# Optimization experiments

Measured on AMD Instinct MI355X. Metric: run time of the kernel, lower is better.

The kernel has to match this reference:

```python
import jax, jax.numpy as jnp
import numpy as np

NODE_NUM = 65536
HID = 256
NUM_CLASS = 64
N_TAB0, N_TAB1 = 40000, 30000
S0, S1 = 8, 4


def setup_inputs() -> dict:
    key = jax.random.key(0)
    ks = jax.random.split(key, 9)
    scale = 1.0 / np.sqrt(HID)
    return {
        "h0": jax.random.normal(ks[0], (NODE_NUM, HID), jnp.float32),
        "tab0": jax.random.normal(ks[1], (N_TAB0, HID), jnp.float32),
        "tab1": jax.random.normal(ks[2], (N_TAB1, HID), jnp.float32),
        "idx0": jax.random.randint(ks[3], (NODE_NUM, S0), 0, N_TAB0, jnp.int32),
        "idx1": jax.random.randint(ks[4], (NODE_NUM, S1), 0, N_TAB1, jnp.int32),
        "W1": jax.random.normal(ks[5], (HID, HID), jnp.float32) * scale,
        "b1": jnp.zeros((HID,), jnp.float32),
        "W2": jax.random.normal(ks[6], (HID, NUM_CLASS), jnp.float32) * scale,
        "b2": jnp.zeros((NUM_CLASS,), jnp.float32),
        "alpha": jax.random.normal(ks[7], (NODE_NUM, 1), jnp.float32),
    }


def _mlp(x, W1, b1, W2, b2):
    # MLP2 with num_layers=2, dropout=0 (eval): relu(x@W1+b1)@W2+b2
    h = jax.nn.relu(jnp.einsum("...i,ij->...j", x, W1) + b1)
    return jnp.einsum("...h,hc->...c", h, W2) + b2


def reference(h0, tab0, tab1, idx0, idx1, W1, b1, W2, b2, alpha):
    # per-type: gather sampled neighbor embeds, MLP, exp(log_softmax)=softmax, mean over samples
    def one_type(tab, idx):
        emb = tab[idx]                                  # [N, S, HID] irregular gather
        cls = jax.nn.softmax(_mlp(emb, W1, b1, W2, b2), axis=-1)  # [N, S, C]
        return jnp.mean(cls, axis=1)                    # [N, C]

    nei_cls = 0.5 * (one_type(tab0, idx0) + one_type(tab1, idx1))
    node_cls = jax.nn.softmax(_mlp(h0, W1, b1, W2, b2), axis=-1)  # [N, C]
    a = jax.nn.sigmoid(alpha)                          # sigmoid(-alpha) = 1 - sigmoid(alpha)
    return a * node_cls + (1.0 - a) * nei_cls
```

## Files before the change

### kernel.cpp

```cpp
#include <hip/hip_runtime.h>

#define HID 256
#define NCLS 64
#define N_NODE 65536
#define N_TAB0 40000
#define N_TAB1 30000
#define S0 8
#define S1 4
#define TILES 2
#define TOTROWS (N_TAB0 + N_TAB1 + N_NODE)
#define PBUF 16384

typedef __attribute__((ext_vector_type(8))) _Float16 f16x8;
typedef __attribute__((ext_vector_type(4))) float f32x4;

__device__ __forceinline__ unsigned short f32_to_h(float x) {
  _Float16 h = (_Float16)x;
  return __builtin_bit_cast(unsigned short, h);
}
__device__ __forceinline__ unsigned pack2h(float lo, float hi) {
  return (unsigned)f32_to_h(lo) | ((unsigned)f32_to_h(hi) << 16);
}

__global__ void prep_kernel(const float* __restrict__ W1, const float* __restrict__ W2,
                            unsigned short* __restrict__ w1f, unsigned short* __restrict__ w2f) {
  int t = blockIdx.x * blockDim.x + threadIdx.x;
  if (t < HID * HID) {
    int j = t & 7, l = (t >> 3) & 63, kt = (t >> 9) & 7, nt = t >> 12;
    w1f[t] = f32_to_h(W1[(kt * 32 + (l >> 4) * 8 + j) * HID + nt * 16 + (l & 15)]);
  } else {
    int t2 = t - HID * HID;
    if (t2 < HID * NCLS) {
      int j = t2 & 7, l = (t2 >> 3) & 63, kt = (t2 >> 9) & 7, ct = t2 >> 12;
      w2f[t2] = f32_to_h(W2[(kt * 32 + (l >> 4) * 8 + j) * NCLS + ct * 16 + (l & 15)]);
    }
  }
}

__launch_bounds__(256, 2)
__global__ void mlp_all_kernel(const float* __restrict__ tab0, const float* __restrict__ tab1,
                               const float* __restrict__ h0,
                               const unsigned short* __restrict__ w1f,
                               const float* __restrict__ b1,
                               const unsigned short* __restrict__ w2f,
                               const float* __restrict__ b2,
                               float* __restrict__ cls0, float* __restrict__ cls1,
                               float* __restrict__ out,
                               const float* __restrict__ alpha) {
  __shared__ __align__(16) char Wlds[2 * PBUF];

  const int t = threadIdx.x;
  const int lane = t & 63;
  const int wv = t >> 6;
  const int nr = lane & 15;
  const int u = lane >> 4;
  const int base = (blockIdx.x * 4 + wv) * (TILES * 16);
  const int lo16 = lane * 16;

  auto STAGE = [&](int pair, int bsel) {
    char* dst = Wlds + bsel * PBUF;
#pragma unroll
    for (int i = 0; i < 4; ++i) {
      const int q = wv * 4 + i;
      const unsigned short* src = w1f + (size_t)(pair * 16 + q) * 512;
      __builtin_amdgcn_global_load_lds(
          (const __attribute__((address_space(1))) void*)(src + lane * 8),
          (__attribute__((address_space(3))) void*)(dst + q * 1024), 16, 0, 0);
    }
  };

  STAGE(0, 0);

  f16x8 bx[TILES][8];
#pragma unroll
  for (int tl = 0; tl < TILES; ++tl) {
    const int row = base + tl * 16 + nr;
    const float* src;
    int lrow;
    if (row < N_TAB0) { src = tab0; lrow = row; }
    else if (row < N_TAB0 + N_TAB1) { src = tab1; lrow = row - N_TAB0; }
    else { src = h0; lrow = row - (N_TAB0 + N_TAB1); }
    const bool rok = (row < TOTROWS);
    const float* xrow = src + (size_t)lrow * HID;
#pragma unroll
    for (int kt = 0; kt < 8; ++kt) {
      float xv[8];
      if (rok) {
        float4 a = *(const float4*)&xrow[kt * 32 + u * 8];
        float4 b = *(const float4*)&xrow[kt * 32 + u * 8 + 4];
        xv[0] = a.x; xv[1] = a.y; xv[2] = a.z; xv[3] = a.w;
        xv[4] = b.x; xv[5] = b.y; xv[6] = b.z; xv[7] = b.w;
      } else {
#pragma unroll
        for (int j = 0; j < 8; ++j) xv[j] = 0.f;
      }
      f16x8 pk;
#pragma unroll
      for (int j = 0; j < 8; ++j) pk[j] = (_Float16)xv[j];
      bx[tl][kt] = pk;
    }
  }

  f32x4 lg[TILES][4];
#pragma unroll
  for (int ct = 0; ct < 4; ++ct) {
    float4 bv = *(const float4*)&b2[ct * 16 + u * 4];
#pragma unroll
    for (int tl = 0; tl < TILES; ++tl) {
      lg[tl][ct][0] = bv.x; lg[tl][ct][1] = bv.y;
      lg[tl][ct][2] = bv.z; lg[tl][ct][3] = bv.w;
    }
  }

  const f16x8* W2F = (const f16x8*)w2f;

  int addr[4];
#pragma unroll
  for (int m = 0; m < 4; ++m) addr[m] = (nr + 16 * (2 * (u & 1) + (m >> 1))) * 4;
  const bool useOdd = (u >= 2);

  auto slice = [&](int nt, unsigned* P0, unsigned* P1) {
    const char* wb = Wlds + ((nt >> 1) & 1) * PBUF + (nt & 1) * 8192;
    f32x4 ae[TILES], ao[TILES];
    float4 bv = *(const float4*)&b1[nt * 16 + u * 4];
#pragma unroll
    for (int tl = 0; tl < TILES; ++tl) {
      ae[tl][0] = bv.x; ae[tl][1] = bv.y; ae[tl][2] = bv.z; ae[tl][3] = bv.w;
      ao[tl][0] = 0.f;  ao[tl][1] = 0.f;  ao[tl][2] = 0.f;  ao[tl][3] = 0.f;
    }
#pragma unroll
    for (int kt = 0; kt < 8; kt += 2) {
      f16x8 ah0 = *(const f16x8*)(wb + kt * 1024 + lo16);
      f16x8 ah1 = *(const f16x8*)(wb + (kt + 1) * 1024 + lo16);
#pragma unroll
      for (int tl = 0; tl < TILES; ++tl) {
        ae[tl] = __builtin_amdgcn_mfma_f32_16x16x32_f16(ah0, bx[tl][kt], ae[tl], 0, 0, 0);
        ao[tl] = __builtin_amdgcn_mfma_f32_16x16x32_f16(ah1, bx[tl][kt + 1], ao[tl], 0, 0, 0);
      }
    }
#pragma unroll
    for (int tl = 0; tl < TILES; ++tl) {
      P0[tl] = pack2h(fmaxf(ae[tl][0] + ao[tl][0], 0.f), fmaxf(ae[tl][1] + ao[tl][1], 0.f));
      P1[tl] = pack2h(fmaxf(ae[tl][2] + ao[tl][2], 0.f), fmaxf(ae[tl][3] + ao[tl][3], 0.f));
    }
  };

  __syncthreads();

  for (int kt2 = 0; kt2 < 8; ++kt2) {
    if (kt2 + 1 < 8) STAGE(kt2 + 1, (kt2 + 1) & 1);

    f16x8 aw[4];
#pragma unroll
    for (int ct = 0; ct < 4; ++ct) aw[ct] = W2F[(ct * 8 + kt2) * 64 + lane];

    unsigned E0[TILES], E1[TILES], O0[TILES], O1[TILES];
    slice(kt2 * 2, E0, E1);
    slice(kt2 * 2 + 1, O0, O1);

    f16x8 bh[TILES];
#pragma unroll
    for (int tl = 0; tl < TILES; ++tl) {
      union { unsigned d[4]; f16x8 v; } r;
#pragma unroll
      for (int m = 0; m < 4; ++m) {
        int e = __builtin_amdgcn_ds_bpermute(addr[m], (int)((m & 1) ? E1[tl] : E0[tl]));
        int o = __builtin_amdgcn_ds_bpermute(addr[m], (int)((m & 1) ? O1[tl] : O0[tl]));
        r.d[m] = (unsigned)(useOdd ? o : e);
      }
      bh[tl] = r.v;
    }

#pragma unroll
    for (int ct = 0; ct < 4; ++ct) {
#pragma unroll
      for (int tl = 0; tl < TILES; ++tl) {
        lg[tl][ct] = __builtin_amdgcn_mfma_f32_16x16x32_f16(aw[ct], bh[tl], lg[tl][ct], 0, 0, 0);
      }
    }

    if (kt2 + 1 < 8) __syncthreads();
  }

#pragma unroll
  for (int tl = 0; tl < TILES; ++tl) {
    const int row = base + tl * 16 + nr;
    float m = lg[tl][0][0];
#pragma unroll
    for (int ct = 0; ct < 4; ++ct)
#pragma unroll
      for (int r = 0; r < 4; ++r) m = fmaxf(m, lg[tl][ct][r]);
    m = fmaxf(m, __shfl_xor(m, 16, 64));
    m = fmaxf(m, __shfl_xor(m, 32, 64));
    float p[4][4];
    float s = 0.f;
#pragma unroll
    for (int ct = 0; ct < 4; ++ct)
#pragma unroll
      for (int r = 0; r < 4; ++r) { p[ct][r] = __expf(lg[tl][ct][r] - m); s += p[ct][r]; }
    s += __shfl_xor(s, 16, 64);
    s += __shfl_xor(s, 32, 64);
    float inv = 1.f / s;

    float* dst;
    int lrow;
    if (row < N_TAB0) { dst = cls0; lrow = row; }
    else if (row < N_TAB0 + N_TAB1) { dst = cls1; lrow = row - N_TAB0; }
    else {
      dst = out; lrow = row - (N_TAB0 + N_TAB1);
      if (row < TOTROWS) inv *= 1.f / (1.f + __expf(-alpha[lrow]));
    }

    if (row < TOTROWS) {
#pragma unroll
      for (int ct = 0; ct < 4; ++ct) {
        float4 o;
        o.x = p[ct][0] * inv; o.y = p[ct][1] * inv;
        o.z = p[ct][2] * inv; o.w = p[ct][3] * inv;
        *(float4*)&dst[(size_t)lrow * NCLS + ct * 16 + u * 4] = o;
      }
    }
  }
}

__launch_bounds__(256)
__global__ void blend_kernel(const float* __restrict__ cls0, const float* __restrict__ cls1,
                             const int* __restrict__ idx0, const int* __restrict__ idx1,
                             const float* __restrict__ alpha, float* __restrict__ out) {
  const int t = threadIdx.x;
  const int lane = t & 63;
  const int wv = t >> 6;
  const int g = lane >> 4;
  const int q = lane & 15;
  const int n = blockIdx.x * 16 + wv * 4 + g;

  int4 ia = *(const int4*)&idx0[n * S0];
  int4 ib = *(const int4*)&idx0[n * S0 + 4];
  int4 ic = *(const int4*)&idx1[n * S1];
  const int j0[S0] = {ia.x, ia.y, ia.z, ia.w, ib.x, ib.y, ib.z, ib.w};
  const int j1[S1] = {ic.x, ic.y, ic.z, ic.w};

  float4 s0 = make_float4(0.f, 0.f, 0.f, 0.f);
#pragma unroll
  for (int k = 0; k < S0; ++k) {
    float4 gv = *(const float4*)&cls0[(size_t)j0[k] * NCLS + q * 4];
    s0.x += gv.x; s0.y += gv.y; s0.z += gv.z; s0.w += gv.w;
  }
  float4 s1 = make_float4(0.f, 0.f, 0.f, 0.f);
#pragma unroll
  for (int k = 0; k < S1; ++k) {
    float4 gv = *(const float4*)&cls1[(size_t)j1[k] * NCLS + q * 4];
    s1.x += gv.x; s1.y += gv.y; s1.z += gv.z; s1.w += gv.w;
  }

  const float a = 1.f / (1.f + __expf(-alpha[n]));
  const float w = (1.f - a) * 0.5f;
  const float c0 = w * (1.f / S0);
  const float c1 = w * (1.f / S1);

  float* op = &out[(size_t)n * NCLS + q * 4];
  float4 o = *(const float4*)op;
  o.x += c0 * s0.x + c1 * s1.x;
  o.y += c0 * s0.y + c1 * s1.y;
  o.z += c0 * s0.z + c1 * s1.z;
  o.w += c0 * s0.w + c1 * s1.w;
  *(float4*)op = o;
}

extern "C" void kernel_launch(void* const* d_in, const int* in_sizes, int n_in,
                              void* d_out, int out_size, void* d_ws, size_t ws_size,
                              hipStream_t stream) {
  const float* h0    = (const float*)d_in[0];
  const float* tab0  = (const float*)d_in[1];
  const float* tab1  = (const float*)d_in[2];
  const int*   idx0  = (const int*)d_in[3];
  const int*   idx1  = (const int*)d_in[4];
  const float* W1    = (const float*)d_in[5];
  const float* b1    = (const float*)d_in[6];
  const float* W2    = (const float*)d_in[7];
  const float* b2    = (const float*)d_in[8];
  const float* alpha = (const float*)d_in[9];
  float* out = (float*)d_out;

  char* ws = (char*)d_ws;
  float* cls0 = (float*)ws;
  float* cls1 = (float*)(ws + 10240000);
  unsigned short* w1f = (unsigned short*)(ws + 17920000);
  unsigned short* w2f = (unsigned short*)(ws + 18051072);

  prep_kernel<<<(HID * HID + HID * NCLS) / 256, 256, 0, stream>>>(W1, W2, w1f, w2f);

  const int RPB = 4 * TILES * 16;
  mlp_all_kernel<<<(TOTROWS + RPB - 1) / RPB, 256, 0, stream>>>(
      tab0, tab1, h0, w1f, b1, w2f, b2, cls0, cls1, out, alpha);

  blend_kernel<<<N_NODE / 16, 256, 0, stream>>>(cls0, cls1, idx0, idx1, alpha, out);
}
```

Before: 90.39 us.

## Stage full W1 in LDS once per 1024-thread block, drop double-buffered pipeline

The MLP kernel now uses 1024-thread blocks with 16 waves, each handling one 16-row tile. The whole fp16 W1 (128 KB) is loaded into LDS once up front, replacing the per-step double-buffered staging and the barriers inside the loop. The goal is to spread each W1 load over more rows and remove the barrier after every step. In exchange, each wave keeps only one tile of rows, so fewer MFMAs run per LDS weight read. The 128 KB of LDS also limits residency to one block per CU, and no loads overlap the compute.

```diff
diff --git a/kernel.cpp b/kernel.cpp
--- a/kernel.cpp
+++ b/kernel.cpp
@@ -7,9 +7,9 @@
 #define N_TAB1 30000
 #define S0 8
 #define S1 4
-#define TILES 2
+#define WAVES 16
+#define TILES 1
 #define TOTROWS (N_TAB0 + N_TAB1 + N_NODE)
-#define PBUF 16384
 
 typedef __attribute__((ext_vector_type(8))) _Float16 f16x8;
 typedef __attribute__((ext_vector_type(4))) float f32x4;
@@ -37,7 +37,7 @@
   }
 }
 
-__launch_bounds__(256, 2)
+__launch_bounds__(1024, 1)
 __global__ void mlp_all_kernel(const float* __restrict__ tab0, const float* __restrict__ tab1,
                                const float* __restrict__ h0,
                                const unsigned short* __restrict__ w1f,
@@ -47,34 +47,27 @@
                                float* __restrict__ cls0, float* __restrict__ cls1,
                                float* __restrict__ out,
                                const float* __restrict__ alpha) {
-  __shared__ __align__(16) char Wlds[2 * PBUF];
+  __shared__ __align__(16) char Wlds[131072];
 
   const int t = threadIdx.x;
   const int lane = t & 63;
   const int wv = t >> 6;
   const int nr = lane & 15;
   const int u = lane >> 4;
-  const int base = (blockIdx.x * 4 + wv) * (TILES * 16);
+  const int base = (blockIdx.x * WAVES + wv) * 16;
   const int lo16 = lane * 16;
 
-  auto STAGE = [&](int pair, int bsel) {
-    char* dst = Wlds + bsel * PBUF;
-#pragma unroll
-    for (int i = 0; i < 4; ++i) {
-      const int q = wv * 4 + i;
-      const unsigned short* src = w1f + (size_t)(pair * 16 + q) * 512;
-      __builtin_amdgcn_global_load_lds(
-          (const __attribute__((address_space(1))) void*)(src + lane * 8),
-          (__attribute__((address_space(3))) void*)(dst + q * 1024), 16, 0, 0);
-    }
-  };
-
-  STAGE(0, 0);
-
-  f16x8 bx[TILES][8];
-#pragma unroll
-  for (int tl = 0; tl < TILES; ++tl) {
-    const int row = base + tl * 16 + nr;
+#pragma unroll
+  for (int i = 0; i < 8; ++i) {
+    const int q = wv * 8 + i;
+    __builtin_amdgcn_global_load_lds(
+        (const __attribute__((address_space(1))) void*)(w1f + (size_t)q * 512 + lane * 8),
+        (__attribute__((address_space(3))) void*)(Wlds + q * 1024), 16, 0, 0);
+  }
+
+  f16x8 bx[8];
+  {
+    const int row = base + nr;
     const float* src;
     int lrow;
     if (row < N_TAB0) { src = tab0; lrow = row; }
@@ -97,19 +90,15 @@
       f16x8 pk;
 #pragma unroll
       for (int j = 0; j < 8; ++j) pk[j] = (_Float16)xv[j];
-      bx[tl][kt] = pk;
-    }
-  }
-
-  f32x4 lg[TILES][4];
+      bx[kt] = pk;
+    }
+  }
+
+  f32x4 lg[4];
 #pragma unroll
   for (int ct = 0; ct < 4; ++ct) {
     float4 bv = *(const float4*)&b2[ct * 16 + u * 4];
-#pragma unroll
-    for (int tl = 0; tl < TILES; ++tl) {
-      lg[tl][ct][0] = bv.x; lg[tl][ct][1] = bv.y;
-      lg[tl][ct][2] = bv.z; lg[tl][ct][3] = bv.w;
-    }
+    lg[ct][0] = bv.x; lg[ct][1] = bv.y; lg[ct][2] = bv.z; lg[ct][3] = bv.w;
   }
 
   const f16x8* W2F = (const f16x8*)w2f;
@@ -120,76 +109,58 @@
   const bool useOdd = (u >= 2);
 
   auto slice = [&](int nt, unsigned* P0, unsigned* P1) {
-    const char* wb = Wlds + ((nt >> 1) & 1) * PBUF + (nt & 1) * 8192;
-    f32x4 ae[TILES], ao[TILES];
+    const char* wb = Wlds + nt * 8192;
+    f32x4 ae, ao;
     float4 bv = *(const float4*)&b1[nt * 16 + u * 4];
-#pragma unroll
-    for (int tl = 0; tl < TILES; ++tl) {
-      ae[tl][0] = bv.x; ae[tl][1] = bv.y; ae[tl][2] = bv.z; ae[tl][3] = bv.w;
-      ao[tl][0] = 0.f;  ao[tl][1] = 0.f;  ao[tl][2] = 0.f;  ao[tl][3] = 0.f;
-    }
+    ae[0] = bv.x; ae[1] = bv.y; ae[2] = bv.z; ae[3] = bv.w;
+    ao[0] = 0.f;  ao[1] = 0.f;  ao[2] = 0.f;  ao[3] = 0.f;
 #pragma unroll
     for (int kt = 0; kt < 8; kt += 2) {
       f16x8 ah0 = *(const f16x8*)(wb + kt * 1024 + lo16);
       f16x8 ah1 = *(const f16x8*)(wb + (kt + 1) * 1024 + lo16);
-#pragma unroll
-      for (int tl = 0; tl < TILES; ++tl) {
-        ae[tl] = __builtin_amdgcn_mfma_f32_16x16x32_f16(ah0, bx[tl][kt], ae[tl], 0, 0, 0);
-        ao[tl] = __builtin_amdgcn_mfma_f32_16x16x32_f16(ah1, bx[tl][kt + 1], ao[tl], 0, 0, 0);
-      }
-    }
-#pragma unroll
-    for (int tl = 0; tl < TILES; ++tl) {
-      P0[tl] = pack2h(fmaxf(ae[tl][0] + ao[tl][0], 0.f), fmaxf(ae[tl][1] + ao[tl][1], 0.f));
-      P1[tl] = pack2h(fmaxf(ae[tl][2] + ao[tl][2], 0.f), fmaxf(ae[tl][3] + ao[tl][3], 0.f));
-    }
+      ae = __builtin_amdgcn_mfma_f32_16x16x32_f16(ah0, bx[kt], ae, 0, 0, 0);
+      ao = __builtin_amdgcn_mfma_f32_16x16x32_f16(ah1, bx[kt + 1], ao, 0, 0, 0);
+    }
+    *P0 = pack2h(fmaxf(ae[0] + ao[0], 0.f), fmaxf(ae[1] + ao[1], 0.f));
+    *P1 = pack2h(fmaxf(ae[2] + ao[2], 0.f), fmaxf(ae[3] + ao[3], 0.f));
   };
 
   __syncthreads();
 
   for (int kt2 = 0; kt2 < 8; ++kt2) {
-    if (kt2 + 1 < 8) STAGE(kt2 + 1, (kt2 + 1) & 1);
-
     f16x8 aw[4];
 #pragma unroll
     for (int ct = 0; ct < 4; ++ct) aw[ct] = W2F[(ct * 8 + kt2) * 64 + lane];
 
-    unsigned E0[TILES], E1[TILES], O0[TILES], O1[TILES];
-    slice(kt2 * 2, E0, E1);
-    slice(kt2 * 2 + 1, O0, O1);
-
-    f16x8 bh[TILES];
-#pragma unroll
-    for (int tl = 0; tl < TILES; ++tl) {
+    unsigned E0, E1, O0, O1;
+    slice(kt2 * 2, &E0, &E1);
+    slice(kt2 * 2 + 1, &O0, &O1);
+
+    f16x8 bh;
+    {
       union { unsigned d[4]; f16x8 v; } r;
 #pragma unroll
       for (int m = 0; m < 4; ++m) {
-        int e = __builtin_amdgcn_ds_bpermute(addr[m], (int)((m & 1) ? E1[tl] : E0[tl]));
-        int o = __builtin_amdgcn_ds_bpermute(addr[m], (int)((m & 1) ? O1[tl] : O0[tl]));
+        int e = __builtin_amdgcn_ds_bpermute(addr[m], (int)((m & 1) ? E1 : E0));
+        int o = __builtin_amdgcn_ds_bpermute(addr[m], (int)((m & 1) ? O1 : O0));
         r.d[m] = (unsigned)(useOdd ? o : e);
       }
-      bh[tl] = r.v;
+      bh = r.v;
     }
 
 #pragma unroll
     for (int ct = 0; ct < 4; ++ct) {
-#pragma unroll
-      for (int tl = 0; tl < TILES; ++tl) {
-        lg[tl][ct] = __builtin_amdgcn_mfma_f32_16x16x32_f16(aw[ct], bh[tl], lg[tl][ct], 0, 0, 0);
-      }
-    }
-
-    if (kt2 + 1 < 8) __syncthreads();
-  }
-
-#pragma unroll
-  for (int tl = 0; tl < TILES; ++tl) {
-    const int row = base + tl * 16 + nr;
-    float m = lg[tl][0][0];
+      lg[ct] = __builtin_amdgcn_mfma_f32_16x16x32_f16(aw[ct], bh, lg[ct], 0, 0, 0);
+    }
+  }
+
+  {
+    const int row = base + nr;
+    float m = lg[0][0];
 #pragma unroll
     for (int ct = 0; ct < 4; ++ct)
 #pragma unroll
-      for (int r = 0; r < 4; ++r) m = fmaxf(m, lg[tl][ct][r]);
+      for (int r = 0; r < 4; ++r) m = fmaxf(m, lg[ct][r]);
     m = fmaxf(m, __shfl_xor(m, 16, 64));
     m = fmaxf(m, __shfl_xor(m, 32, 64));
     float p[4][4];
@@ -197,7 +168,7 @@
 #pragma unroll
     for (int ct = 0; ct < 4; ++ct)
 #pragma unroll
-      for (int r = 0; r < 4; ++r) { p[ct][r] = __expf(lg[tl][ct][r] - m); s += p[ct][r]; }
+      for (int r = 0; r < 4; ++r) { p[ct][r] = __expf(lg[ct][r] - m); s += p[ct][r]; }
     s += __shfl_xor(s, 16, 64);
     s += __shfl_xor(s, 32, 64);
     float inv = 1.f / s;
@@ -290,8 +261,8 @@
 
   prep_kernel<<<(HID * HID + HID * NCLS) / 256, 256, 0, stream>>>(W1, W2, w1f, w2f);
 
-  const int RPB = 4 * TILES * 16;
-  mlp_all_kernel<<<(TOTROWS + RPB - 1) / RPB, 256, 0, stream>>>(
+  const int RPB = WAVES * TILES * 16;
+  mlp_all_kernel<<<(TOTROWS + RPB - 1) / RPB, 1024, 0, stream>>>(
       tab0, tab1, h0, w1f, b1, w2f, b2, cls0, cls1, out, alpha);
 
   blend_kernel<<<N_NODE / 16, 256, 0, stream>>>(cls0, cls1, idx0, idx1, alpha, out);
```

Measured after the change: 106.6 us. 1.18x slower.

## Stage W1 in four-slice groups and issue bpermutes between slice MFMAs

Applied to the files above, without the earlier changes.

W1 is now staged into LDS in groups of four 16-column slices, using two 32KB buffers instead of two 16KB ones. This halves the number of block-wide barriers in the main loop and fully unrolls it. The even-slice ds_bpermute shuffles are issued before the odd-slice MFMAs so the LDS permute latency can overlap with matrix work. The cost is doubled LDS (64KB per block), which may limit occupancy against the 2-blocks-per-CU launch bound, and extra register pressure from the unrolling.

```diff
diff --git a/kernel.cpp b/kernel.cpp
--- a/kernel.cpp
+++ b/kernel.cpp
@@ -9,7 +9,7 @@
 #define S1 4
 #define TILES 2
 #define TOTROWS (N_TAB0 + N_TAB1 + N_NODE)
-#define PBUF 16384
+#define QBUF 32768
 
 typedef __attribute__((ext_vector_type(8))) _Float16 f16x8;
 typedef __attribute__((ext_vector_type(4))) float f32x4;
@@ -47,7 +47,7 @@
                                float* __restrict__ cls0, float* __restrict__ cls1,
                                float* __restrict__ out,
                                const float* __restrict__ alpha) {
-  __shared__ __align__(16) char Wlds[2 * PBUF];
+  __shared__ __align__(16) char Wlds[2 * QBUF];
 
   const int t = threadIdx.x;
   const int lane = t & 63;
@@ -57,19 +57,19 @@
   const int base = (blockIdx.x * 4 + wv) * (TILES * 16);
   const int lo16 = lane * 16;
 
-  auto STAGE = [&](int pair, int bsel) {
-    char* dst = Wlds + bsel * PBUF;
-#pragma unroll
-    for (int i = 0; i < 4; ++i) {
-      const int q = wv * 4 + i;
-      const unsigned short* src = w1f + (size_t)(pair * 16 + q) * 512;
+  auto STAGE4 = [&](int grp, int bsel) {
+    char* dst = Wlds + bsel * QBUF;
+#pragma unroll
+    for (int i = 0; i < 8; ++i) {
+      const int q = wv * 8 + i;
+      const unsigned short* src = w1f + (size_t)(grp * 32 + q) * 512;
       __builtin_amdgcn_global_load_lds(
           (const __attribute__((address_space(1))) void*)(src + lane * 8),
           (__attribute__((address_space(3))) void*)(dst + q * 1024), 16, 0, 0);
     }
   };
 
-  STAGE(0, 0);
+  STAGE4(0, 0);
 
   f16x8 bx[TILES][8];
 #pragma unroll
@@ -120,7 +120,7 @@
   const bool useOdd = (u >= 2);
 
   auto slice = [&](int nt, unsigned* P0, unsigned* P1) {
-    const char* wb = Wlds + ((nt >> 1) & 1) * PBUF + (nt & 1) * 8192;
+    const char* wb = Wlds + ((nt >> 2) & 1) * QBUF + (nt & 3) * 8192;
     f32x4 ae[TILES], ao[TILES];
     float4 bv = *(const float4*)&b1[nt * 16 + u * 4];
 #pragma unroll
@@ -147,39 +147,55 @@
 
   __syncthreads();
 
-  for (int kt2 = 0; kt2 < 8; ++kt2) {
-    if (kt2 + 1 < 8) STAGE(kt2 + 1, (kt2 + 1) & 1);
-
-    f16x8 aw[4];
-#pragma unroll
-    for (int ct = 0; ct < 4; ++ct) aw[ct] = W2F[(ct * 8 + kt2) * 64 + lane];
-
-    unsigned E0[TILES], E1[TILES], O0[TILES], O1[TILES];
-    slice(kt2 * 2, E0, E1);
-    slice(kt2 * 2 + 1, O0, O1);
-
-    f16x8 bh[TILES];
-#pragma unroll
-    for (int tl = 0; tl < TILES; ++tl) {
-      union { unsigned d[4]; f16x8 v; } r;
-#pragma unroll
-      for (int m = 0; m < 4; ++m) {
-        int e = __builtin_amdgcn_ds_bpermute(addr[m], (int)((m & 1) ? E1[tl] : E0[tl]));
-        int o = __builtin_amdgcn_ds_bpermute(addr[m], (int)((m & 1) ? O1[tl] : O0[tl]));
-        r.d[m] = (unsigned)(useOdd ? o : e);
-      }
-      bh[tl] = r.v;
-    }
-
-#pragma unroll
-    for (int ct = 0; ct < 4; ++ct) {
+#pragma unroll
+  for (int g = 0; g < 4; ++g) {
+    if (g + 1 < 4) STAGE4(g + 1, (g + 1) & 1);
+
+#pragma unroll
+    for (int h = 0; h < 2; ++h) {
+      const int kt2 = g * 2 + h;
+
+      f16x8 aw[4];
+#pragma unroll
+      for (int ct = 0; ct < 4; ++ct) aw[ct] = W2F[(ct * 8 + kt2) * 64 + lane];
+
+      unsigned E0[TILES], E1[TILES], O0[TILES], O1[TILES];
+      slice(kt2 * 2, E0, E1);
+
+      int eb[TILES][4];
+#pragma unroll
+      for (int tl = 0; tl < TILES; ++tl)
+#pragma unroll
+        for (int m = 0; m < 4; ++m)
+          eb[tl][m] = __builtin_amdgcn_ds_bpermute(addr[m], (int)((m & 1) ? E1[tl] : E0[tl]));
+
+      slice(kt2 * 2 + 1, O0, O1);
+
+      int ob[TILES][4];
+#pragma unroll
+      for (int tl = 0; tl < TILES; ++tl)
+#pragma unroll
+        for (int m = 0; m < 4; ++m)
+          ob[tl][m] = __builtin_amdgcn_ds_bpermute(addr[m], (int)((m & 1) ? O1[tl] : O0[tl]));
+
+      f16x8 bh[TILES];
 #pragma unroll
       for (int tl = 0; tl < TILES; ++tl) {
-        lg[tl][ct] = __builtin_amdgcn_mfma_f32_16x16x32_f16(aw[ct], bh[tl], lg[tl][ct], 0, 0, 0);
-      }
-    }
-
-    if (kt2 + 1 < 8) __syncthreads();
+        union { unsigned d[4]; f16x8 v; } r;
+#pragma unroll
+        for (int m = 0; m < 4; ++m) r.d[m] = (unsigned)(useOdd ? ob[tl][m] : eb[tl][m]);
+        bh[tl] = r.v;
+      }
+#pragma unroll
+      for (int ct = 0; ct < 4; ++ct) {
+#pragma unroll
+        for (int tl = 0; tl < TILES; ++tl) {
+          lg[tl][ct] = __builtin_amdgcn_mfma_f32_16x16x32_f16(aw[ct], bh[tl], lg[tl][ct], 0, 0, 0);
+        }
+      }
+    }
+
+    if (g + 1 < 4) __syncthreads();
   }
 
 #pragma unroll
```

After: 94.90 us. 1.05x slower.
